# Kernel tuning notes

Hardware: AMD Instinct MI355X
Metric: run time of the kernel (lower is better)

Reference implementation:

```python
import jax, jax.numpy as jnp
import numpy as np

N_NODES = 50000
N_EDGES = 800000


def gcn_conv(x, edge_index, W, b):
    """PyG GCNConv: add self-loops, symmetric deg^{-1/2} normalization,
    dense transform, scatter-add aggregation."""
    n = x.shape[0]
    src, dst = edge_index[0], edge_index[1]
    # add self-loops
    loop = jnp.arange(n, dtype=src.dtype)
    src = jnp.concatenate([src, loop])
    dst = jnp.concatenate([dst, loop])
    # degree on destination nodes (includes self-loops -> deg >= 1)
    deg = jax.ops.segment_sum(jnp.ones_like(dst, dtype=x.dtype), dst, num_segments=n)
    dinv = jax.lax.rsqrt(deg)
    norm = dinv[src] * dinv[dst]  # [E+N]
    h = x @ W                     # [N, F_out] dense GEMM
    msg = h[src] * norm[:, None]  # gather + scale, [E+N, F_out]
    out = jax.ops.segment_sum(msg, dst, num_segments=n)  # scatter-add
    return out + b


def setup_inputs() -> dict:
    key = jax.random.key(0)
    ks = jax.random.split(key, 8)
    x = jax.random.normal(ks[0], (N_NODES, 100), dtype=jnp.float32)
    edge_index = jax.random.randint(ks[1], (2, N_EDGES), 0, N_NODES, dtype=jnp.int64)
    W1 = jax.random.normal(ks[2], (100, 256), dtype=jnp.float32) * 0.1
    b1 = jnp.zeros((256,), dtype=jnp.float32)
    W2 = jax.random.normal(ks[3], (256, 128), dtype=jnp.float32) * 0.06
    b2 = jnp.zeros((128,), dtype=jnp.float32)
    Wfc = jax.random.normal(ks[4], (128, 1), dtype=jnp.float32) * 0.09
    bfc = jnp.zeros((1,), dtype=jnp.float32)
    return {"x": x, "edge_index": edge_index, "W1": W1, "b1": b1,
            "W2": W2, "b2": b2, "Wfc": Wfc, "bfc": bfc}


def reference(x, edge_index, W1, b1, W2, b2, Wfc, bfc):
    # eval mode: F.dropout with training=False is identity
    h = jax.nn.relu(gcn_conv(x, edge_index, W1, b1))
    h = jax.nn.relu(gcn_conv(h, edge_index, W2, b2))
    return h @ Wfc + bfc  # [N, 1]
```

## Files before the change

### kernel.cpp

```cpp
#include <hip/hip_runtime.h>
#include <hip/hip_bf16.h>


#define F0 100
#define F1 256
#define F2 128


__global__ void zero_i32(int* p, int n) {
    int i = blockIdx.x * blockDim.x + threadIdx.x;
    if (i < n) p[i] = 0;
}

__global__ void deg_count_i(const int* __restrict__ dst, int* deg, int e) {
    int i = blockIdx.x * blockDim.x + threadIdx.x;
    if (i < e) atomicAdd(deg + dst[i], 1);
}

__global__ __launch_bounds__(256) void scan1(const int* __restrict__ deg,
                                             int* __restrict__ excl,
                                             int* __restrict__ bsum,
                                             float* __restrict__ dinv, int n) {
    __shared__ int wsum[4];
    int i = blockIdx.x * 256 + threadIdx.x;
    int lane = threadIdx.x & 63, wid = threadIdx.x >> 6;
    int v = (i < n) ? deg[i] : 0;
    if (i < n) dinv[i] = rsqrtf((float)(v + 1));
    int s = v;
#pragma unroll
    for (int off = 1; off < 64; off <<= 1) {
        int t = __shfl_up(s, off, 64);
        if (lane >= off) s += t;
    }
    if (lane == 63) wsum[wid] = s;
    __syncthreads();
    int add = 0;
    for (int w = 0; w < wid; w++) add += wsum[w];
    if (i < n) excl[i] = add + s - v;
    if (threadIdx.x == 255) bsum[blockIdx.x] = add + s;
}

__global__ __launch_bounds__(256) void scan2(int* __restrict__ bsum, int nb,
                                             int* __restrict__ rowptr, int n) {
    __shared__ int wsum[4];
    int lane = threadIdx.x & 63, wid = threadIdx.x >> 6;
    int v = (threadIdx.x < nb) ? bsum[threadIdx.x] : 0;
    int s = v;
#pragma unroll
    for (int off = 1; off < 64; off <<= 1) {
        int t = __shfl_up(s, off, 64);
        if (lane >= off) s += t;
    }
    if (lane == 63) wsum[wid] = s;
    __syncthreads();
    int add = 0;
    for (int w = 0; w < wid; w++) add += wsum[w];
    if (threadIdx.x < nb) bsum[threadIdx.x] = add + s - v;
    if (threadIdx.x == 255) rowptr[n] = add + s;
}

__global__ void scan3(const int* __restrict__ excl, const int* __restrict__ bsum,
                      int* __restrict__ rowptr, int* __restrict__ cursor, int n) {
    int i = blockIdx.x * 256 + threadIdx.x;
    if (i < n) {
        int r = excl[i] + bsum[blockIdx.x];
        rowptr[i] = r;
        cursor[i] = r;
    }
}

__global__ void csr_fill(const int* __restrict__ src, const int* __restrict__ dst,
                         int* cursor, int* __restrict__ csr, int e) {
    int i = blockIdx.x * blockDim.x + threadIdx.x;
    if (i < e) {
        int pos = atomicAdd(cursor + dst[i], 1);
        csr[pos] = src[i];
    }
}

__global__ void scale_x(const float4* __restrict__ x4,
                        const float* __restrict__ dinv,
                        float4* __restrict__ xs4, int n25) {
    int i = blockIdx.x * blockDim.x + threadIdx.x;
    if (i < n25) {
        float d = dinv[i / 25];
        float4 v = x4[i];
        v.x *= d; v.y *= d; v.z *= d; v.w *= d;
        xs4[i] = v;
    }
}


__global__ __launch_bounds__(256) void pull_f100(
        const float* __restrict__ xs, const int* __restrict__ rowptr,
        const int* __restrict__ csr, const float* __restrict__ dinv,
        float* __restrict__ agg, int n) {
    int wave = threadIdx.x >> 6, lane = threadIdx.x & 63;
    int v = blockIdx.x * 4 + wave;
    if (v >= n) return;
    int beg = rowptr[v], end = rowptr[v + 1];
    float dv = dinv[v];
    int half = lane >> 5, q = lane & 31;
    bool act = q < 25;
    float4 acc = {0.f, 0.f, 0.f, 0.f};
    if (half == 0 && act) acc = ((const float4*)(xs + (size_t)v * F0))[q];

    for (int base = beg; base < end; base += 64) {
        int cnt = min(64, end - base);
        int sidx = (lane < cnt) ? csr[base + lane] : 0;
        int npf = cnt >> 1;
        int p = 0;
        for (; p + 4 <= npf; p += 4) {
            int s0 = __shfl(sidx, 2 * p + half, 64);
            int s1 = __shfl(sidx, 2 * p + 2 + half, 64);
            int s2 = __shfl(sidx, 2 * p + 4 + half, 64);
            int s3 = __shfl(sidx, 2 * p + 6 + half, 64);
            if (act) {
                float4 r0 = ((const float4*)(xs + (size_t)s0 * F0))[q];
                float4 r1 = ((const float4*)(xs + (size_t)s1 * F0))[q];
                float4 r2 = ((const float4*)(xs + (size_t)s2 * F0))[q];
                float4 r3 = ((const float4*)(xs + (size_t)s3 * F0))[q];
                acc.x += (r0.x + r1.x) + (r2.x + r3.x);
                acc.y += (r0.y + r1.y) + (r2.y + r3.y);
                acc.z += (r0.z + r1.z) + (r2.z + r3.z);
                acc.w += (r0.w + r1.w) + (r2.w + r3.w);
            }
        }
        for (; p < npf; p++) {
            int s0 = __shfl(sidx, 2 * p + half, 64);
            if (act) {
                float4 r0 = ((const float4*)(xs + (size_t)s0 * F0))[q];
                acc.x += r0.x; acc.y += r0.y; acc.z += r0.z; acc.w += r0.w;
            }
        }
        if (cnt & 1) {
            int sl = __shfl(sidx, cnt - 1, 64);
            if (half == 0 && act) {
                float4 r = ((const float4*)(xs + (size_t)sl * F0))[q];
                acc.x += r.x; acc.y += r.y; acc.z += r.z; acc.w += r.w;
            }
        }
    }
    float ox = __shfl_down(acc.x, 32, 64);
    float oy = __shfl_down(acc.y, 32, 64);
    float oz = __shfl_down(acc.z, 32, 64);
    float ow = __shfl_down(acc.w, 32, 64);
    if (half == 0 && act) {
        float4 r;
        r.x = dv * (acc.x + ox);
        r.y = dv * (acc.y + oy);
        r.z = dv * (acc.z + oz);
        r.w = dv * (acc.w + ow);
        ((float4*)(agg + (size_t)v * F0))[q] = r;
    }
}

__global__ __launch_bounds__(256) void pull_f128_fused(
        const float* __restrict__ h2s, const int* __restrict__ rowptr,
        const int* __restrict__ csr, const float* __restrict__ dinv,
        const float* __restrict__ b2, const float* __restrict__ Wfc,
        const float* __restrict__ bfc, float* __restrict__ out, int n) {
    int wave = threadIdx.x >> 6, lane = threadIdx.x & 63;
    int v = blockIdx.x * 4 + wave;
    if (v >= n) return;
    int beg = rowptr[v], end = rowptr[v + 1];
    float dv = dinv[v];
    int half = lane >> 5, q = lane & 31;
    float4 acc = {0.f, 0.f, 0.f, 0.f};
    if (half == 0) acc = ((const float4*)(h2s + (size_t)v * F2))[q];

    for (int base = beg; base < end; base += 64) {
        int cnt = min(64, end - base);
        int sidx = (lane < cnt) ? csr[base + lane] : 0;
        int npf = cnt >> 1;
        int p = 0;
        for (; p + 4 <= npf; p += 4) {
            int s0 = __shfl(sidx, 2 * p + half, 64);
            int s1 = __shfl(sidx, 2 * p + 2 + half, 64);
            int s2 = __shfl(sidx, 2 * p + 4 + half, 64);
            int s3 = __shfl(sidx, 2 * p + 6 + half, 64);
            float4 r0 = ((const float4*)(h2s + (size_t)s0 * F2))[q];
            float4 r1 = ((const float4*)(h2s + (size_t)s1 * F2))[q];
            float4 r2 = ((const float4*)(h2s + (size_t)s2 * F2))[q];
            float4 r3 = ((const float4*)(h2s + (size_t)s3 * F2))[q];
            acc.x += (r0.x + r1.x) + (r2.x + r3.x);
            acc.y += (r0.y + r1.y) + (r2.y + r3.y);
            acc.z += (r0.z + r1.z) + (r2.z + r3.z);
            acc.w += (r0.w + r1.w) + (r2.w + r3.w);
        }
        for (; p < npf; p++) {
            int s0 = __shfl(sidx, 2 * p + half, 64);
            float4 r0 = ((const float4*)(h2s + (size_t)s0 * F2))[q];
            acc.x += r0.x; acc.y += r0.y; acc.z += r0.z; acc.w += r0.w;
        }
        if (cnt & 1) {
            int sl = __shfl(sidx, cnt - 1, 64);
            if (half == 0) {
                float4 r = ((const float4*)(h2s + (size_t)sl * F2))[q];
                acc.x += r.x; acc.y += r.y; acc.z += r.z; acc.w += r.w;
            }
        }
    }
    float ox = __shfl_down(acc.x, 32, 64);
    float oy = __shfl_down(acc.y, 32, 64);
    float oz = __shfl_down(acc.z, 32, 64);
    float ow = __shfl_down(acc.w, 32, 64);
    if (half == 0) {
        float4 b2v = ((const float4*)b2)[q];
        float4 wv = ((const float4*)Wfc)[q];
        float t0 = dv * (acc.x + ox);
        float t1 = dv * (acc.y + oy);
        float t2 = dv * (acc.z + oz);
        float t3 = dv * (acc.w + ow);
        float part = fmaxf(t0 + b2v.x, 0.f) * wv.x + fmaxf(t1 + b2v.y, 0.f) * wv.y +
                     fmaxf(t2 + b2v.z, 0.f) * wv.z + fmaxf(t3 + b2v.w, 0.f) * wv.w;
        part += __shfl_down(part, 16, 64);
        part += __shfl_down(part, 8, 64);
        part += __shfl_down(part, 4, 64);
        part += __shfl_down(part, 2, 64);
        part += __shfl_down(part, 1, 64);
        if (lane == 0) out[v] = part + bfc[0];
    }
}


__global__ __launch_bounds__(256) void gemm1_tiled(
        const float* __restrict__ A, const float* __restrict__ W,
        const float* __restrict__ bias, float* __restrict__ C, int n) {
    __shared__ float As[20 * 128];
    __shared__ float Bs[20 * 128];
    int tid = threadIdx.x;
    int r0 = blockIdx.x * 128;
    int c0 = blockIdx.y * 128;
    int tc = tid & 15, tr = tid >> 4;
    float acc[8][8] = {};

    for (int k0 = 0; k0 < F0; k0 += 20) {
        if (k0) __syncthreads();
        for (int idx = tid; idx < 128 * 5; idx += 256) {
            int row = idx & 127, kq = idx >> 7;
            int gr = r0 + row;
            if (gr >= n) gr = n - 1;
            float4 v = *(const float4*)(A + (size_t)gr * F0 + k0 + 4 * kq);
            As[(4 * kq + 0) * 128 + row] = v.x;
            As[(4 * kq + 1) * 128 + row] = v.y;
            As[(4 * kq + 2) * 128 + row] = v.z;
            As[(4 * kq + 3) * 128 + row] = v.w;
        }
        for (int idx = tid; idx < 20 * 32; idx += 256) {
            int k = idx >> 5, cq = idx & 31;
            *(float4*)(Bs + k * 128 + 4 * cq) =
                *(const float4*)(W + (size_t)(k0 + k) * F1 + c0 + 4 * cq);
        }
        __syncthreads();
#pragma unroll 5
        for (int k = 0; k < 20; k++) {
            float4 a0 = *(const float4*)(As + k * 128 + 4 * tr);
            float4 a1 = *(const float4*)(As + k * 128 + 64 + 4 * tr);
            float4 b0 = *(const float4*)(Bs + k * 128 + 4 * tc);
            float4 b1 = *(const float4*)(Bs + k * 128 + 64 + 4 * tc);
            float av[8] = {a0.x, a0.y, a0.z, a0.w, a1.x, a1.y, a1.z, a1.w};
            float bv[8] = {b0.x, b0.y, b0.z, b0.w, b1.x, b1.y, b1.z, b1.w};
#pragma unroll
            for (int i = 0; i < 8; i++)
#pragma unroll
                for (int j = 0; j < 8; j++) acc[i][j] += av[i] * bv[j];
        }
    }
    float4 bb0 = *(const float4*)(bias + c0 + 4 * tc);
    float4 bb1 = *(const float4*)(bias + c0 + 64 + 4 * tc);
    float bv[8] = {bb0.x, bb0.y, bb0.z, bb0.w, bb1.x, bb1.y, bb1.z, bb1.w};
#pragma unroll
    for (int i = 0; i < 8; i++) {
        int row = (i < 4) ? (4 * tr + i) : (64 + 4 * tr + i - 4);
        int gr = r0 + row;
        if (gr < n) {
            float4 o0, o1;
            o0.x = fmaxf(acc[i][0] + bv[0], 0.f);
            o0.y = fmaxf(acc[i][1] + bv[1], 0.f);
            o0.z = fmaxf(acc[i][2] + bv[2], 0.f);
            o0.w = fmaxf(acc[i][3] + bv[3], 0.f);
            o1.x = fmaxf(acc[i][4] + bv[4], 0.f);
            o1.y = fmaxf(acc[i][5] + bv[5], 0.f);
            o1.z = fmaxf(acc[i][6] + bv[6], 0.f);
            o1.w = fmaxf(acc[i][7] + bv[7], 0.f);
            *(float4*)(C + (size_t)gr * F1 + c0 + 4 * tc) = o0;
            *(float4*)(C + (size_t)gr * F1 + c0 + 64 + 4 * tc) = o1;
        }
    }
}

__global__ __launch_bounds__(256) void gemm2_tiled(
        const float* __restrict__ A, const float* __restrict__ W,
        const float* __restrict__ dinv, float* __restrict__ C, int n) {
    __shared__ float As[32 * 64];
    __shared__ float Bs[32 * 128];
    int tid = threadIdx.x;
    int r0 = blockIdx.x * 64;
    int tc = tid & 15, tr = tid >> 4;
    float acc[4][8] = {};

    for (int k0 = 0; k0 < F1; k0 += 32) {
        if (k0) __syncthreads();
        for (int idx = tid; idx < 64 * 8; idx += 256) {
            int row = idx & 63, kq = idx >> 6;
            int gr = r0 + row;
            if (gr >= n) gr = n - 1;
            float4 v = *(const float4*)(A + (size_t)gr * F1 + k0 + 4 * kq);
            As[(4 * kq + 0) * 64 + row] = v.x;
            As[(4 * kq + 1) * 64 + row] = v.y;
            As[(4 * kq + 2) * 64 + row] = v.z;
            As[(4 * kq + 3) * 64 + row] = v.w;
        }
        for (int idx = tid; idx < 32 * 32; idx += 256) {
            int k = idx >> 5, cq = idx & 31;
            *(float4*)(Bs + k * 128 + 4 * cq) =
                *(const float4*)(W + (size_t)(k0 + k) * F2 + 4 * cq);
        }
        __syncthreads();
#pragma unroll 4
        for (int k = 0; k < 32; k++) {
            float4 a = *(const float4*)(As + k * 64 + 4 * tr);
            float4 b0 = *(const float4*)(Bs + k * 128 + 4 * tc);
            float4 b1 = *(const float4*)(Bs + k * 128 + 64 + 4 * tc);
            float av[4] = {a.x, a.y, a.z, a.w};
            float bv[8] = {b0.x, b0.y, b0.z, b0.w, b1.x, b1.y, b1.z, b1.w};
#pragma unroll
            for (int i = 0; i < 4; i++)
#pragma unroll
                for (int j = 0; j < 8; j++) acc[i][j] += av[i] * bv[j];
        }
    }
#pragma unroll
    for (int i = 0; i < 4; i++) {
        int gr = r0 + 4 * tr + i;
        if (gr < n) {
            float d = dinv[gr];
            float4 o0 = {acc[i][0] * d, acc[i][1] * d, acc[i][2] * d, acc[i][3] * d};
            float4 o1 = {acc[i][4] * d, acc[i][5] * d, acc[i][6] * d, acc[i][7] * d};
            *(float4*)(C + (size_t)gr * F2 + 4 * tc) = o0;
            *(float4*)(C + (size_t)gr * F2 + 64 + 4 * tc) = o1;
        }
    }
}


static inline size_t align16(size_t x) { return (x + 3) & ~(size_t)3; }

extern "C" void kernel_launch(void* const* d_in, const int* in_sizes, int n_in,
                              void* d_out, int out_size, void* d_ws, size_t ws_size,
                              hipStream_t stream) {
    const float* x   = (const float*)d_in[0];
    const int*   ei  = (const int*)d_in[1];
    const float* W1  = (const float*)d_in[2];
    const float* b1  = (const float*)d_in[3];
    const float* W2  = (const float*)d_in[4];
    const float* b2  = (const float*)d_in[5];
    const float* Wfc = (const float*)d_in[6];
    const float* bfc = (const float*)d_in[7];
    float* out = (float*)d_out;

    const int n = in_sizes[0] / F0;
    const int e = in_sizes[1] / 2;
    const int* src = ei;
    const int* dst = ei + e;

    char* wsb = (char*)d_ws;
    size_t off = 0;
    int* deg    = (int*)(wsb + 4 * off); off = align16(off + n);
    int* excl   = (int*)(wsb + 4 * off); off = align16(off + n);
    int* bsum   = (int*)(wsb + 4 * off); off = align16(off + 256);
    int* rowptr = (int*)(wsb + 4 * off); off = align16(off + n + 1);
    int* cursor = (int*)(wsb + 4 * off); off = align16(off + n);
    int* csr    = (int*)(wsb + 4 * off); off = align16(off + e);
    float* dinv = (float*)(wsb + 4 * off); off = align16(off + n);
    float* xs   = (float*)(wsb + 4 * off); off = align16(off + (size_t)n * F0);
    float* aggX = (float*)(wsb + 4 * off); off = align16(off + (size_t)n * F0);
    float* a1   = (float*)(wsb + 4 * off); off = align16(off + (size_t)n * F1);
    float* h2s  = (float*)(wsb + 4 * off); off = align16(off + (size_t)n * F2);

    const int B = 256;
    const int nb = (n + B - 1) / B;

    zero_i32<<<nb, B, 0, stream>>>(deg, n);
    deg_count_i<<<(e + B - 1) / B, B, 0, stream>>>(dst, deg, e);
    scan1<<<nb, B, 0, stream>>>(deg, excl, bsum, dinv, n);
    scale_x<<<((n * 25) + B - 1) / B, B, 0, stream>>>(
        (const float4*)x, dinv, (float4*)xs, n * 25);
    scan2<<<1, B, 0, stream>>>(bsum, nb, rowptr, n);
    scan3<<<nb, B, 0, stream>>>(excl, bsum, rowptr, cursor, n);
    csr_fill<<<(e + B - 1) / B, B, 0, stream>>>(src, dst, cursor, csr, e);

    pull_f100<<<(n + 3) / 4, 256, 0, stream>>>(xs, rowptr, csr, dinv, aggX, n);
    gemm1_tiled<<<dim3((n + 127) / 128, F1 / 128), 256, 0, stream>>>(
        aggX, W1, b1, a1, n);

    gemm2_tiled<<<(n + 63) / 64, 256, 0, stream>>>(a1, W2, dinv, h2s, n);
    pull_f128_fused<<<(n + 3) / 4, 256, 0, stream>>>(h2s, rowptr, csr, dinv,
                                                     b2, Wfc, bfc, out, n);
}
```

Baseline: 392.0 us.

## Split gather tables into column halves to shrink per-pass working set

The scaled input features and the layer-2 hidden features are now written as two column-split tables (52/48 and 64/64 floats per row). Each aggregation runs as two passes, one per half, with 16 lanes per neighbor and 4 neighbors in flight per wave. The aim is a gathered table small enough to stay resident in the last-level cache during random neighbor gathers. In exchange the CSR is traversed twice, there are two extra launches, and the final FC output is accumulated across two kernels with a read-modify-write.

```diff
diff --git a/kernel.cpp b/kernel.cpp
--- a/kernel.cpp
+++ b/kernel.cpp
@@ -78,148 +78,127 @@
     }
 }
 
-__global__ void scale_x(const float4* __restrict__ x4,
-                        const float* __restrict__ dinv,
-                        float4* __restrict__ xs4, int n25) {
+__global__ void scale_x_split(const float4* __restrict__ x4,
+                              const float* __restrict__ dinv,
+                              float4* __restrict__ xsA, float4* __restrict__ xsB,
+                              int n) {
     int i = blockIdx.x * blockDim.x + threadIdx.x;
-    if (i < n25) {
-        float d = dinv[i / 25];
+    if (i < n * 25) {
+        int row = i / 25, kq = i - row * 25;
+        float d = dinv[row];
         float4 v = x4[i];
         v.x *= d; v.y *= d; v.z *= d; v.w *= d;
-        xs4[i] = v;
-    }
-}
-
-
-__global__ __launch_bounds__(256) void pull_f100(
-        const float* __restrict__ xs, const int* __restrict__ rowptr,
+        if (kq < 13) xsA[row * 13 + kq] = v;
+        else         xsB[row * 12 + (kq - 13)] = v;
+    }
+}
+
+
+template <int NQ>
+__global__ __launch_bounds__(256) void pull_q_agg(
+        const float* __restrict__ xtab, const int* __restrict__ rowptr,
         const int* __restrict__ csr, const float* __restrict__ dinv,
-        float* __restrict__ agg, int n) {
+        float* __restrict__ agg, int c0, int n) {
     int wave = threadIdx.x >> 6, lane = threadIdx.x & 63;
     int v = blockIdx.x * 4 + wave;
     if (v >= n) return;
     int beg = rowptr[v], end = rowptr[v + 1];
     float dv = dinv[v];
-    int half = lane >> 5, q = lane & 31;
-    bool act = q < 25;
+    int g = lane >> 4, q = lane & 15;
+    bool act = q < NQ;
     float4 acc = {0.f, 0.f, 0.f, 0.f};
-    if (half == 0 && act) acc = ((const float4*)(xs + (size_t)v * F0))[q];
+    if (g == 0 && act) acc = ((const float4*)(xtab + (size_t)v * (4 * NQ)))[q];
 
     for (int base = beg; base < end; base += 64) {
         int cnt = min(64, end - base);
         int sidx = (lane < cnt) ? csr[base + lane] : 0;
-        int npf = cnt >> 1;
-        int p = 0;
-        for (; p + 4 <= npf; p += 4) {
-            int s0 = __shfl(sidx, 2 * p + half, 64);
-            int s1 = __shfl(sidx, 2 * p + 2 + half, 64);
-            int s2 = __shfl(sidx, 2 * p + 4 + half, 64);
-            int s3 = __shfl(sidx, 2 * p + 6 + half, 64);
+        int nq = cnt >> 2;
+        for (int p = 0; p < nq; p++) {
+            int s = __shfl(sidx, 4 * p + g, 64);
             if (act) {
-                float4 r0 = ((const float4*)(xs + (size_t)s0 * F0))[q];
-                float4 r1 = ((const float4*)(xs + (size_t)s1 * F0))[q];
-                float4 r2 = ((const float4*)(xs + (size_t)s2 * F0))[q];
-                float4 r3 = ((const float4*)(xs + (size_t)s3 * F0))[q];
-                acc.x += (r0.x + r1.x) + (r2.x + r3.x);
-                acc.y += (r0.y + r1.y) + (r2.y + r3.y);
-                acc.z += (r0.z + r1.z) + (r2.z + r3.z);
-                acc.w += (r0.w + r1.w) + (r2.w + r3.w);
-            }
-        }
-        for (; p < npf; p++) {
-            int s0 = __shfl(sidx, 2 * p + half, 64);
-            if (act) {
-                float4 r0 = ((const float4*)(xs + (size_t)s0 * F0))[q];
-                acc.x += r0.x; acc.y += r0.y; acc.z += r0.z; acc.w += r0.w;
-            }
-        }
-        if (cnt & 1) {
-            int sl = __shfl(sidx, cnt - 1, 64);
-            if (half == 0 && act) {
-                float4 r = ((const float4*)(xs + (size_t)sl * F0))[q];
+                float4 r = ((const float4*)(xtab + (size_t)s * (4 * NQ)))[q];
                 acc.x += r.x; acc.y += r.y; acc.z += r.z; acc.w += r.w;
             }
         }
-    }
-    float ox = __shfl_down(acc.x, 32, 64);
-    float oy = __shfl_down(acc.y, 32, 64);
-    float oz = __shfl_down(acc.z, 32, 64);
-    float ow = __shfl_down(acc.w, 32, 64);
-    if (half == 0 && act) {
-        float4 r;
-        r.x = dv * (acc.x + ox);
-        r.y = dv * (acc.y + oy);
-        r.z = dv * (acc.z + oz);
-        r.w = dv * (acc.w + ow);
-        ((float4*)(agg + (size_t)v * F0))[q] = r;
-    }
-}
-
-__global__ __launch_bounds__(256) void pull_f128_fused(
-        const float* __restrict__ h2s, const int* __restrict__ rowptr,
+        int rem = cnt & 3;
+        if (rem) {
+            int s = __shfl(sidx, 4 * nq + g, 64);
+            if (g < rem && act) {
+                float4 r = ((const float4*)(xtab + (size_t)s * (4 * NQ)))[q];
+                acc.x += r.x; acc.y += r.y; acc.z += r.z; acc.w += r.w;
+            }
+        }
+    }
+    acc.x += __shfl_down(acc.x, 32, 64);
+    acc.y += __shfl_down(acc.y, 32, 64);
+    acc.z += __shfl_down(acc.z, 32, 64);
+    acc.w += __shfl_down(acc.w, 32, 64);
+    acc.x += __shfl_down(acc.x, 16, 64);
+    acc.y += __shfl_down(acc.y, 16, 64);
+    acc.z += __shfl_down(acc.z, 16, 64);
+    acc.w += __shfl_down(acc.w, 16, 64);
+    if (g == 0 && act) {
+        float4 r = {dv * acc.x, dv * acc.y, dv * acc.z, dv * acc.w};
+        *(float4*)(agg + (size_t)v * F0 + c0 + 4 * q) = r;
+    }
+}
+
+template <int ADD>
+__global__ __launch_bounds__(256) void pull_h64_fc(
+        const float* __restrict__ htab, const int* __restrict__ rowptr,
         const int* __restrict__ csr, const float* __restrict__ dinv,
-        const float* __restrict__ b2, const float* __restrict__ Wfc,
+        const float* __restrict__ b2h, const float* __restrict__ Wfch,
         const float* __restrict__ bfc, float* __restrict__ out, int n) {
     int wave = threadIdx.x >> 6, lane = threadIdx.x & 63;
     int v = blockIdx.x * 4 + wave;
     if (v >= n) return;
     int beg = rowptr[v], end = rowptr[v + 1];
     float dv = dinv[v];
-    int half = lane >> 5, q = lane & 31;
+    int g = lane >> 4, q = lane & 15;
     float4 acc = {0.f, 0.f, 0.f, 0.f};
-    if (half == 0) acc = ((const float4*)(h2s + (size_t)v * F2))[q];
+    if (g == 0) acc = ((const float4*)(htab + (size_t)v * 64))[q];
 
     for (int base = beg; base < end; base += 64) {
         int cnt = min(64, end - base);
         int sidx = (lane < cnt) ? csr[base + lane] : 0;
-        int npf = cnt >> 1;
-        int p = 0;
-        for (; p + 4 <= npf; p += 4) {
-            int s0 = __shfl(sidx, 2 * p + half, 64);
-            int s1 = __shfl(sidx, 2 * p + 2 + half, 64);
-            int s2 = __shfl(sidx, 2 * p + 4 + half, 64);
-            int s3 = __shfl(sidx, 2 * p + 6 + half, 64);
-            float4 r0 = ((const float4*)(h2s + (size_t)s0 * F2))[q];
-            float4 r1 = ((const float4*)(h2s + (size_t)s1 * F2))[q];
-            float4 r2 = ((const float4*)(h2s + (size_t)s2 * F2))[q];
-            float4 r3 = ((const float4*)(h2s + (size_t)s3 * F2))[q];
-            acc.x += (r0.x + r1.x) + (r2.x + r3.x);
-            acc.y += (r0.y + r1.y) + (r2.y + r3.y);
-            acc.z += (r0.z + r1.z) + (r2.z + r3.z);
-            acc.w += (r0.w + r1.w) + (r2.w + r3.w);
-        }
-        for (; p < npf; p++) {
-            int s0 = __shfl(sidx, 2 * p + half, 64);
-            float4 r0 = ((const float4*)(h2s + (size_t)s0 * F2))[q];
-            acc.x += r0.x; acc.y += r0.y; acc.z += r0.z; acc.w += r0.w;
-        }
-        if (cnt & 1) {
-            int sl = __shfl(sidx, cnt - 1, 64);
-            if (half == 0) {
-                float4 r = ((const float4*)(h2s + (size_t)sl * F2))[q];
+        int nq = cnt >> 2;
+        for (int p = 0; p < nq; p++) {
+            int s = __shfl(sidx, 4 * p + g, 64);
+            float4 r = ((const float4*)(htab + (size_t)s * 64))[q];
+            acc.x += r.x; acc.y += r.y; acc.z += r.z; acc.w += r.w;
+        }
+        int rem = cnt & 3;
+        if (rem) {
+            int s = __shfl(sidx, 4 * nq + g, 64);
+            if (g < rem) {
+                float4 r = ((const float4*)(htab + (size_t)s * 64))[q];
                 acc.x += r.x; acc.y += r.y; acc.z += r.z; acc.w += r.w;
             }
         }
     }
-    float ox = __shfl_down(acc.x, 32, 64);
-    float oy = __shfl_down(acc.y, 32, 64);
-    float oz = __shfl_down(acc.z, 32, 64);
-    float ow = __shfl_down(acc.w, 32, 64);
-    if (half == 0) {
-        float4 b2v = ((const float4*)b2)[q];
-        float4 wv = ((const float4*)Wfc)[q];
-        float t0 = dv * (acc.x + ox);
-        float t1 = dv * (acc.y + oy);
-        float t2 = dv * (acc.z + oz);
-        float t3 = dv * (acc.w + ow);
-        float part = fmaxf(t0 + b2v.x, 0.f) * wv.x + fmaxf(t1 + b2v.y, 0.f) * wv.y +
-                     fmaxf(t2 + b2v.z, 0.f) * wv.z + fmaxf(t3 + b2v.w, 0.f) * wv.w;
-        part += __shfl_down(part, 16, 64);
+    acc.x += __shfl_down(acc.x, 32, 64);
+    acc.y += __shfl_down(acc.y, 32, 64);
+    acc.z += __shfl_down(acc.z, 32, 64);
+    acc.w += __shfl_down(acc.w, 32, 64);
+    acc.x += __shfl_down(acc.x, 16, 64);
+    acc.y += __shfl_down(acc.y, 16, 64);
+    acc.z += __shfl_down(acc.z, 16, 64);
+    acc.w += __shfl_down(acc.w, 16, 64);
+    if (lane < 16) {
+        float4 b = ((const float4*)b2h)[q];
+        float4 w = ((const float4*)Wfch)[q];
+        float part = fmaxf(dv * acc.x + b.x, 0.f) * w.x +
+                     fmaxf(dv * acc.y + b.y, 0.f) * w.y +
+                     fmaxf(dv * acc.z + b.z, 0.f) * w.z +
+                     fmaxf(dv * acc.w + b.w, 0.f) * w.w;
         part += __shfl_down(part, 8, 64);
         part += __shfl_down(part, 4, 64);
         part += __shfl_down(part, 2, 64);
         part += __shfl_down(part, 1, 64);
-        if (lane == 0) out[v] = part + bfc[0];
+        if (lane == 0) {
+            if (ADD) out[v] += part + bfc[0];
+            else     out[v] = part;
+        }
     }
 }
 
@@ -292,7 +271,8 @@
 
 __global__ __launch_bounds__(256) void gemm2_tiled(
         const float* __restrict__ A, const float* __restrict__ W,
-        const float* __restrict__ dinv, float* __restrict__ C, int n) {
+        const float* __restrict__ dinv, float* __restrict__ h2sA,
+        float* __restrict__ h2sB, int n) {
     __shared__ float As[32 * 64];
     __shared__ float Bs[32 * 128];
     int tid = threadIdx.x;
@@ -338,8 +318,8 @@
             float d = dinv[gr];
             float4 o0 = {acc[i][0] * d, acc[i][1] * d, acc[i][2] * d, acc[i][3] * d};
             float4 o1 = {acc[i][4] * d, acc[i][5] * d, acc[i][6] * d, acc[i][7] * d};
-            *(float4*)(C + (size_t)gr * F2 + 4 * tc) = o0;
-            *(float4*)(C + (size_t)gr * F2 + 64 + 4 * tc) = o1;
+            *(float4*)(h2sA + (size_t)gr * 64 + 4 * tc) = o0;
+            *(float4*)(h2sB + (size_t)gr * 64 + 4 * tc) = o1;
         }
     }
 }
@@ -367,17 +347,19 @@
 
     char* wsb = (char*)d_ws;
     size_t off = 0;
-    int* deg    = (int*)(wsb + 4 * off); off = align16(off + n);
-    int* excl   = (int*)(wsb + 4 * off); off = align16(off + n);
-    int* bsum   = (int*)(wsb + 4 * off); off = align16(off + 256);
-    int* rowptr = (int*)(wsb + 4 * off); off = align16(off + n + 1);
-    int* cursor = (int*)(wsb + 4 * off); off = align16(off + n);
-    int* csr    = (int*)(wsb + 4 * off); off = align16(off + e);
-    float* dinv = (float*)(wsb + 4 * off); off = align16(off + n);
-    float* xs   = (float*)(wsb + 4 * off); off = align16(off + (size_t)n * F0);
-    float* aggX = (float*)(wsb + 4 * off); off = align16(off + (size_t)n * F0);
-    float* a1   = (float*)(wsb + 4 * off); off = align16(off + (size_t)n * F1);
-    float* h2s  = (float*)(wsb + 4 * off); off = align16(off + (size_t)n * F2);
+    int* deg     = (int*)(wsb + 4 * off); off = align16(off + n);
+    int* excl    = (int*)(wsb + 4 * off); off = align16(off + n);
+    int* bsum    = (int*)(wsb + 4 * off); off = align16(off + 256);
+    int* rowptr  = (int*)(wsb + 4 * off); off = align16(off + n + 1);
+    int* cursor  = (int*)(wsb + 4 * off); off = align16(off + n);
+    int* csr     = (int*)(wsb + 4 * off); off = align16(off + e);
+    float* dinv  = (float*)(wsb + 4 * off); off = align16(off + n);
+    float* xsA   = (float*)(wsb + 4 * off); off = align16(off + (size_t)n * 52);
+    float* xsB   = (float*)(wsb + 4 * off); off = align16(off + (size_t)n * 48);
+    float* aggX  = (float*)(wsb + 4 * off); off = align16(off + (size_t)n * F0);
+    float* a1    = (float*)(wsb + 4 * off); off = align16(off + (size_t)n * F1);
+    float* h2sA  = (float*)(wsb + 4 * off); off = align16(off + (size_t)n * 64);
+    float* h2sB  = (float*)(wsb + 4 * off); off = align16(off + (size_t)n * 64);
 
     const int B = 256;
     const int nb = (n + B - 1) / B;
@@ -385,17 +367,21 @@
     zero_i32<<<nb, B, 0, stream>>>(deg, n);
     deg_count_i<<<(e + B - 1) / B, B, 0, stream>>>(dst, deg, e);
     scan1<<<nb, B, 0, stream>>>(deg, excl, bsum, dinv, n);
-    scale_x<<<((n * 25) + B - 1) / B, B, 0, stream>>>(
-        (const float4*)x, dinv, (float4*)xs, n * 25);
+    scale_x_split<<<((n * 25) + B - 1) / B, B, 0, stream>>>(
+        (const float4*)x, dinv, (float4*)xsA, (float4*)xsB, n);
     scan2<<<1, B, 0, stream>>>(bsum, nb, rowptr, n);
     scan3<<<nb, B, 0, stream>>>(excl, bsum, rowptr, cursor, n);
     csr_fill<<<(e + B - 1) / B, B, 0, stream>>>(src, dst, cursor, csr, e);
 
-    pull_f100<<<(n + 3) / 4, 256, 0, stream>>>(xs, rowptr, csr, dinv, aggX, n);
+    const int pgrid = (n + 3) / 4;
+    pull_q_agg<13><<<pgrid, 256, 0, stream>>>(xsA, rowptr, csr, dinv, aggX, 0, n);
+    pull_q_agg<12><<<pgrid, 256, 0, stream>>>(xsB, rowptr, csr, dinv, aggX, 52, n);
     gemm1_tiled<<<dim3((n + 127) / 128, F1 / 128), 256, 0, stream>>>(
         aggX, W1, b1, a1, n);
 
-    gemm2_tiled<<<(n + 63) / 64, 256, 0, stream>>>(a1, W2, dinv, h2s, n);
-    pull_f128_fused<<<(n + 3) / 4, 256, 0, stream>>>(h2s, rowptr, csr, dinv,
-                                                     b2, Wfc, bfc, out, n);
-}
+    gemm2_tiled<<<(n + 63) / 64, 256, 0, stream>>>(a1, W2, dinv, h2sA, h2sB, n);
+    pull_h64_fc<0><<<pgrid, 256, 0, stream>>>(h2sA, rowptr, csr, dinv,
+                                              b2, Wfc, bfc, out, n);
+    pull_h64_fc<1><<<pgrid, 256, 0, stream>>>(h2sB, rowptr, csr, dinv,
+                                              b2 + 64, Wfc + 64, bfc, out, n);
+}
```

Result: slower. 407.1 us (+3.8%).

## Restructure GEMM tiles to row-major shared A with full-K staging

Applied to the files above, without the earlier changes.

gemm1 now uses 64-row tiles with a 4x8 per-thread micro-tile and stages the whole K=100 slice of A and W into shared memory in one pass, removing the K-loop syncs. gemm2 doubles the K-chunk to 64 and stores A row-major with padding (stride 68) instead of transposing it into shared memory. The goal is cheaper, vectorized global-to-shared copies and fewer barriers. The cost is scalar strided shared reads of A in the inner loop, possible bank conflicts (gemm1 has no padding), and lower arithmetic intensity per thread in gemm1.

```diff
diff --git a/kernel.cpp b/kernel.cpp
--- a/kernel.cpp
+++ b/kernel.cpp
@@ -227,53 +227,47 @@
 __global__ __launch_bounds__(256) void gemm1_tiled(
         const float* __restrict__ A, const float* __restrict__ W,
         const float* __restrict__ bias, float* __restrict__ C, int n) {
-    __shared__ float As[20 * 128];
-    __shared__ float Bs[20 * 128];
+    __shared__ float Ax[64 * F0];
+    __shared__ float Bs[F0 * 128];
     int tid = threadIdx.x;
-    int r0 = blockIdx.x * 128;
+    int r0 = blockIdx.x * 64;
     int c0 = blockIdx.y * 128;
     int tc = tid & 15, tr = tid >> 4;
-    float acc[8][8] = {};
-
-    for (int k0 = 0; k0 < F0; k0 += 20) {
-        if (k0) __syncthreads();
-        for (int idx = tid; idx < 128 * 5; idx += 256) {
-            int row = idx & 127, kq = idx >> 7;
-            int gr = r0 + row;
-            if (gr >= n) gr = n - 1;
-            float4 v = *(const float4*)(A + (size_t)gr * F0 + k0 + 4 * kq);
-            As[(4 * kq + 0) * 128 + row] = v.x;
-            As[(4 * kq + 1) * 128 + row] = v.y;
-            As[(4 * kq + 2) * 128 + row] = v.z;
-            As[(4 * kq + 3) * 128 + row] = v.w;
-        }
-        for (int idx = tid; idx < 20 * 32; idx += 256) {
-            int k = idx >> 5, cq = idx & 31;
-            *(float4*)(Bs + k * 128 + 4 * cq) =
-                *(const float4*)(W + (size_t)(k0 + k) * F1 + c0 + 4 * cq);
-        }
-        __syncthreads();
-#pragma unroll 5
-        for (int k = 0; k < 20; k++) {
-            float4 a0 = *(const float4*)(As + k * 128 + 4 * tr);
-            float4 a1 = *(const float4*)(As + k * 128 + 64 + 4 * tr);
-            float4 b0 = *(const float4*)(Bs + k * 128 + 4 * tc);
-            float4 b1 = *(const float4*)(Bs + k * 128 + 64 + 4 * tc);
-            float av[8] = {a0.x, a0.y, a0.z, a0.w, a1.x, a1.y, a1.z, a1.w};
-            float bv[8] = {b0.x, b0.y, b0.z, b0.w, b1.x, b1.y, b1.z, b1.w};
-#pragma unroll
-            for (int i = 0; i < 8; i++)
-#pragma unroll
-                for (int j = 0; j < 8; j++) acc[i][j] += av[i] * bv[j];
-        }
+
+    for (int idx = tid; idx < 64 * 25; idx += 256) {
+        int row = idx / 25, kq = idx - row * 25;
+        int gr = r0 + row;
+        if (gr >= n) gr = n - 1;
+        *(float4*)(Ax + row * F0 + 4 * kq) =
+            *(const float4*)(A + (size_t)gr * F0 + 4 * kq);
+    }
+    for (int idx = tid; idx < F0 * 32; idx += 256) {
+        int k = idx >> 5, cq = idx & 31;
+        *(float4*)(Bs + k * 128 + 4 * cq) =
+            *(const float4*)(W + (size_t)k * F1 + c0 + 4 * cq);
+    }
+    __syncthreads();
+
+    float acc[4][8] = {};
+#pragma unroll 4
+    for (int k = 0; k < F0; k++) {
+        float av[4];
+#pragma unroll
+        for (int i = 0; i < 4; i++) av[i] = Ax[(4 * tr + i) * F0 + k];
+        float4 b0 = *(const float4*)(Bs + k * 128 + 4 * tc);
+        float4 b1 = *(const float4*)(Bs + k * 128 + 64 + 4 * tc);
+        float bv[8] = {b0.x, b0.y, b0.z, b0.w, b1.x, b1.y, b1.z, b1.w};
+#pragma unroll
+        for (int i = 0; i < 4; i++)
+#pragma unroll
+            for (int j = 0; j < 8; j++) acc[i][j] += av[i] * bv[j];
     }
     float4 bb0 = *(const float4*)(bias + c0 + 4 * tc);
     float4 bb1 = *(const float4*)(bias + c0 + 64 + 4 * tc);
     float bv[8] = {bb0.x, bb0.y, bb0.z, bb0.w, bb1.x, bb1.y, bb1.z, bb1.w};
 #pragma unroll
-    for (int i = 0; i < 8; i++) {
-        int row = (i < 4) ? (4 * tr + i) : (64 + 4 * tr + i - 4);
-        int gr = r0 + row;
+    for (int i = 0; i < 4; i++) {
+        int gr = r0 + 4 * tr + i;
         if (gr < n) {
             float4 o0, o1;
             o0.x = fmaxf(acc[i][0] + bv[0], 0.f);
@@ -293,37 +287,35 @@
 __global__ __launch_bounds__(256) void gemm2_tiled(
         const float* __restrict__ A, const float* __restrict__ W,
         const float* __restrict__ dinv, float* __restrict__ C, int n) {
-    __shared__ float As[32 * 64];
-    __shared__ float Bs[32 * 128];
+    __shared__ float Ax[64 * 68];
+    __shared__ float Bs[64 * 128];
     int tid = threadIdx.x;
     int r0 = blockIdx.x * 64;
     int tc = tid & 15, tr = tid >> 4;
     float acc[4][8] = {};
 
-    for (int k0 = 0; k0 < F1; k0 += 32) {
+    for (int k0 = 0; k0 < F1; k0 += 64) {
         if (k0) __syncthreads();
-        for (int idx = tid; idx < 64 * 8; idx += 256) {
-            int row = idx & 63, kq = idx >> 6;
+        for (int idx = tid; idx < 64 * 16; idx += 256) {
+            int kq = idx & 15, row = idx >> 4;
             int gr = r0 + row;
             if (gr >= n) gr = n - 1;
-            float4 v = *(const float4*)(A + (size_t)gr * F1 + k0 + 4 * kq);
-            As[(4 * kq + 0) * 64 + row] = v.x;
-            As[(4 * kq + 1) * 64 + row] = v.y;
-            As[(4 * kq + 2) * 64 + row] = v.z;
-            As[(4 * kq + 3) * 64 + row] = v.w;
-        }
-        for (int idx = tid; idx < 32 * 32; idx += 256) {
+            *(float4*)(Ax + row * 68 + 4 * kq) =
+                *(const float4*)(A + (size_t)gr * F1 + k0 + 4 * kq);
+        }
+        for (int idx = tid; idx < 64 * 32; idx += 256) {
             int k = idx >> 5, cq = idx & 31;
             *(float4*)(Bs + k * 128 + 4 * cq) =
                 *(const float4*)(W + (size_t)(k0 + k) * F2 + 4 * cq);
         }
         __syncthreads();
 #pragma unroll 4
-        for (int k = 0; k < 32; k++) {
-            float4 a = *(const float4*)(As + k * 64 + 4 * tr);
+        for (int k = 0; k < 64; k++) {
+            float av[4];
+#pragma unroll
+            for (int i = 0; i < 4; i++) av[i] = Ax[(4 * tr + i) * 68 + k];
             float4 b0 = *(const float4*)(Bs + k * 128 + 4 * tc);
             float4 b1 = *(const float4*)(Bs + k * 128 + 64 + 4 * tc);
-            float av[4] = {a.x, a.y, a.z, a.w};
             float bv[8] = {b0.x, b0.y, b0.z, b0.w, b1.x, b1.y, b1.z, b1.w};
 #pragma unroll
             for (int i = 0; i < 4; i++)
@@ -381,6 +373,7 @@
 
     const int B = 256;
     const int nb = (n + B - 1) / B;
+    const int rb64 = (n + 63) / 64;
 
     zero_i32<<<nb, B, 0, stream>>>(deg, n);
     deg_count_i<<<(e + B - 1) / B, B, 0, stream>>>(dst, deg, e);
@@ -392,10 +385,9 @@
     csr_fill<<<(e + B - 1) / B, B, 0, stream>>>(src, dst, cursor, csr, e);
 
     pull_f100<<<(n + 3) / 4, 256, 0, stream>>>(xs, rowptr, csr, dinv, aggX, n);
-    gemm1_tiled<<<dim3((n + 127) / 128, F1 / 128), 256, 0, stream>>>(
-        aggX, W1, b1, a1, n);
-
-    gemm2_tiled<<<(n + 63) / 64, 256, 0, stream>>>(a1, W2, dinv, h2s, n);
+    gemm1_tiled<<<dim3(rb64, F1 / 128), 256, 0, stream>>>(aggX, W1, b1, a1, n);
+
+    gemm2_tiled<<<rb64, 256, 0, stream>>>(a1, W2, dinv, h2s, n);
     pull_f128_fused<<<(n + 3) / 4, 256, 0, stream>>>(h2s, rowptr, csr, dinv,
                                                      b2, Wfc, bfc, out, n);
 }
```

New measurement: 397.2 us. Within noise of the previous version (+1.3%).

## Retile both GEMMs to 128-thread blocks with 8x8 contiguous micro-tiles

Applied to the files above, without the earlier changes.

Both dense GEMMs now run with 128-thread blocks over 64-row tiles, and each thread computes an 8x8 block of contiguous rows and columns. gemm1 loads the whole K=100 slice of A and W into shared memory in one pass, which removes the inner K-chunk loop and its barriers. gemm2 doubles per-thread work to 8x8 to get more register reuse. The costs are higher shared memory use in gemm1 (about 75KB per block) and more registers per thread, which may lower occupancy, and the contiguous 8-float LDS reads may cause bank conflicts.

```diff
diff --git a/kernel.cpp b/kernel.cpp
--- a/kernel.cpp
+++ b/kernel.cpp
@@ -224,56 +224,53 @@
 }
 
 
-__global__ __launch_bounds__(256) void gemm1_tiled(
+__global__ __launch_bounds__(128) void gemm1_tiled(
         const float* __restrict__ A, const float* __restrict__ W,
         const float* __restrict__ bias, float* __restrict__ C, int n) {
-    __shared__ float As[20 * 128];
-    __shared__ float Bs[20 * 128];
+    __shared__ float As[F0 * 64];
+    __shared__ float Bs[F0 * 128];
     int tid = threadIdx.x;
-    int r0 = blockIdx.x * 128;
+    int r0 = blockIdx.x * 64;
     int c0 = blockIdx.y * 128;
     int tc = tid & 15, tr = tid >> 4;
+
+    for (int idx = tid; idx < 64 * 25; idx += 128) {
+        int row = idx & 63, kq = idx >> 6;
+        int gr = r0 + row;
+        if (gr >= n) gr = n - 1;
+        float4 v = *(const float4*)(A + (size_t)gr * F0 + 4 * kq);
+        As[(4 * kq + 0) * 64 + row] = v.x;
+        As[(4 * kq + 1) * 64 + row] = v.y;
+        As[(4 * kq + 2) * 64 + row] = v.z;
+        As[(4 * kq + 3) * 64 + row] = v.w;
+    }
+    for (int idx = tid; idx < F0 * 32; idx += 128) {
+        int k = idx >> 5, cq = idx & 31;
+        *(float4*)(Bs + k * 128 + 4 * cq) =
+            *(const float4*)(W + (size_t)k * F1 + c0 + 4 * cq);
+    }
+    __syncthreads();
+
     float acc[8][8] = {};
-
-    for (int k0 = 0; k0 < F0; k0 += 20) {
-        if (k0) __syncthreads();
-        for (int idx = tid; idx < 128 * 5; idx += 256) {
-            int row = idx & 127, kq = idx >> 7;
-            int gr = r0 + row;
-            if (gr >= n) gr = n - 1;
-            float4 v = *(const float4*)(A + (size_t)gr * F0 + k0 + 4 * kq);
-            As[(4 * kq + 0) * 128 + row] = v.x;
-            As[(4 * kq + 1) * 128 + row] = v.y;
-            As[(4 * kq + 2) * 128 + row] = v.z;
-            As[(4 * kq + 3) * 128 + row] = v.w;
-        }
-        for (int idx = tid; idx < 20 * 32; idx += 256) {
-            int k = idx >> 5, cq = idx & 31;
-            *(float4*)(Bs + k * 128 + 4 * cq) =
-                *(const float4*)(W + (size_t)(k0 + k) * F1 + c0 + 4 * cq);
-        }
-        __syncthreads();
-#pragma unroll 5
-        for (int k = 0; k < 20; k++) {
-            float4 a0 = *(const float4*)(As + k * 128 + 4 * tr);
-            float4 a1 = *(const float4*)(As + k * 128 + 64 + 4 * tr);
-            float4 b0 = *(const float4*)(Bs + k * 128 + 4 * tc);
-            float4 b1 = *(const float4*)(Bs + k * 128 + 64 + 4 * tc);
-            float av[8] = {a0.x, a0.y, a0.z, a0.w, a1.x, a1.y, a1.z, a1.w};
-            float bv[8] = {b0.x, b0.y, b0.z, b0.w, b1.x, b1.y, b1.z, b1.w};
-#pragma unroll
-            for (int i = 0; i < 8; i++)
-#pragma unroll
-                for (int j = 0; j < 8; j++) acc[i][j] += av[i] * bv[j];
-        }
-    }
-    float4 bb0 = *(const float4*)(bias + c0 + 4 * tc);
-    float4 bb1 = *(const float4*)(bias + c0 + 64 + 4 * tc);
+#pragma unroll 4
+    for (int k = 0; k < F0; k++) {
+        float4 a0 = *(const float4*)(As + k * 64 + 8 * tr);
+        float4 a1 = *(const float4*)(As + k * 64 + 8 * tr + 4);
+        float4 b0 = *(const float4*)(Bs + k * 128 + 8 * tc);
+        float4 b1 = *(const float4*)(Bs + k * 128 + 8 * tc + 4);
+        float av[8] = {a0.x, a0.y, a0.z, a0.w, a1.x, a1.y, a1.z, a1.w};
+        float bv[8] = {b0.x, b0.y, b0.z, b0.w, b1.x, b1.y, b1.z, b1.w};
+#pragma unroll
+        for (int i = 0; i < 8; i++)
+#pragma unroll
+            for (int j = 0; j < 8; j++) acc[i][j] += av[i] * bv[j];
+    }
+    float4 bb0 = *(const float4*)(bias + c0 + 8 * tc);
+    float4 bb1 = *(const float4*)(bias + c0 + 8 * tc + 4);
     float bv[8] = {bb0.x, bb0.y, bb0.z, bb0.w, bb1.x, bb1.y, bb1.z, bb1.w};
 #pragma unroll
     for (int i = 0; i < 8; i++) {
-        int row = (i < 4) ? (4 * tr + i) : (64 + 4 * tr + i - 4);
-        int gr = r0 + row;
+        int gr = r0 + 8 * tr + i;
         if (gr < n) {
             float4 o0, o1;
             o0.x = fmaxf(acc[i][0] + bv[0], 0.f);
@@ -284,13 +281,13 @@
             o1.y = fmaxf(acc[i][5] + bv[5], 0.f);
             o1.z = fmaxf(acc[i][6] + bv[6], 0.f);
             o1.w = fmaxf(acc[i][7] + bv[7], 0.f);
-            *(float4*)(C + (size_t)gr * F1 + c0 + 4 * tc) = o0;
-            *(float4*)(C + (size_t)gr * F1 + c0 + 64 + 4 * tc) = o1;
-        }
-    }
-}
-
-__global__ __launch_bounds__(256) void gemm2_tiled(
+            *(float4*)(C + (size_t)gr * F1 + c0 + 8 * tc) = o0;
+            *(float4*)(C + (size_t)gr * F1 + c0 + 8 * tc + 4) = o1;
+        }
+    }
+}
+
+__global__ __launch_bounds__(128) void gemm2_tiled(
         const float* __restrict__ A, const float* __restrict__ W,
         const float* __restrict__ dinv, float* __restrict__ C, int n) {
     __shared__ float As[32 * 64];
@@ -298,11 +295,11 @@
     int tid = threadIdx.x;
     int r0 = blockIdx.x * 64;
     int tc = tid & 15, tr = tid >> 4;
-    float acc[4][8] = {};
+    float acc[8][8] = {};
 
     for (int k0 = 0; k0 < F1; k0 += 32) {
         if (k0) __syncthreads();
-        for (int idx = tid; idx < 64 * 8; idx += 256) {
+        for (int idx = tid; idx < 64 * 8; idx += 128) {
             int row = idx & 63, kq = idx >> 6;
             int gr = r0 + row;
             if (gr >= n) gr = n - 1;
@@ -312,7 +309,7 @@
             As[(4 * kq + 2) * 64 + row] = v.z;
             As[(4 * kq + 3) * 64 + row] = v.w;
         }
-        for (int idx = tid; idx < 32 * 32; idx += 256) {
+        for (int idx = tid; idx < 32 * 32; idx += 128) {
             int k = idx >> 5, cq = idx & 31;
             *(float4*)(Bs + k * 128 + 4 * cq) =
                 *(const float4*)(W + (size_t)(k0 + k) * F2 + 4 * cq);
@@ -320,26 +317,27 @@
         __syncthreads();
 #pragma unroll 4
         for (int k = 0; k < 32; k++) {
-            float4 a = *(const float4*)(As + k * 64 + 4 * tr);
-            float4 b0 = *(const float4*)(Bs + k * 128 + 4 * tc);
-            float4 b1 = *(const float4*)(Bs + k * 128 + 64 + 4 * tc);
-            float av[4] = {a.x, a.y, a.z, a.w};
+            float4 a0 = *(const float4*)(As + k * 64 + 8 * tr);
+            float4 a1 = *(const float4*)(As + k * 64 + 8 * tr + 4);
+            float4 b0 = *(const float4*)(Bs + k * 128 + 8 * tc);
+            float4 b1 = *(const float4*)(Bs + k * 128 + 8 * tc + 4);
+            float av[8] = {a0.x, a0.y, a0.z, a0.w, a1.x, a1.y, a1.z, a1.w};
             float bv[8] = {b0.x, b0.y, b0.z, b0.w, b1.x, b1.y, b1.z, b1.w};
 #pragma unroll
-            for (int i = 0; i < 4; i++)
+            for (int i = 0; i < 8; i++)
 #pragma unroll
                 for (int j = 0; j < 8; j++) acc[i][j] += av[i] * bv[j];
         }
     }
 #pragma unroll
-    for (int i = 0; i < 4; i++) {
-        int gr = r0 + 4 * tr + i;
+    for (int i = 0; i < 8; i++) {
+        int gr = r0 + 8 * tr + i;
         if (gr < n) {
             float d = dinv[gr];
             float4 o0 = {acc[i][0] * d, acc[i][1] * d, acc[i][2] * d, acc[i][3] * d};
             float4 o1 = {acc[i][4] * d, acc[i][5] * d, acc[i][6] * d, acc[i][7] * d};
-            *(float4*)(C + (size_t)gr * F2 + 4 * tc) = o0;
-            *(float4*)(C + (size_t)gr * F2 + 64 + 4 * tc) = o1;
+            *(float4*)(C + (size_t)gr * F2 + 8 * tc) = o0;
+            *(float4*)(C + (size_t)gr * F2 + 8 * tc + 4) = o1;
         }
     }
 }
@@ -381,6 +379,7 @@
 
     const int B = 256;
     const int nb = (n + B - 1) / B;
+    const int rb64 = (n + 63) / 64;
 
     zero_i32<<<nb, B, 0, stream>>>(deg, n);
     deg_count_i<<<(e + B - 1) / B, B, 0, stream>>>(dst, deg, e);
@@ -392,10 +391,9 @@
     csr_fill<<<(e + B - 1) / B, B, 0, stream>>>(src, dst, cursor, csr, e);
 
     pull_f100<<<(n + 3) / 4, 256, 0, stream>>>(xs, rowptr, csr, dinv, aggX, n);
-    gemm1_tiled<<<dim3((n + 127) / 128, F1 / 128), 256, 0, stream>>>(
-        aggX, W1, b1, a1, n);
-
-    gemm2_tiled<<<(n + 63) / 64, 256, 0, stream>>>(a1, W2, dinv, h2s, n);
+    gemm1_tiled<<<dim3(rb64, F1 / 128), 128, 0, stream>>>(aggX, W1, b1, a1, n);
+
+    gemm2_tiled<<<rb64, 128, 0, stream>>>(a1, W2, dinv, h2s, n);
     pull_f128_fused<<<(n + 3) / 4, 256, 0, stream>>>(h2s, rowptr, csr, dinv,
                                                      b2, Wfc, bfc, out, n);
 }
```

New measurement: 449.3 us. 14.6% more time.
